# Kernel optimization log

Hardware: AMD Instinct MI355X
Metric: run time of the kernel (lower is better)

The kernel has to match this reference:

```python
import jax, jax.numpy as jnp
import numpy as np

NEG_BIG = -10000000000.0  # value used by masked_fill_ in the original


def setup_inputs() -> dict:
    S, B, H = 2048, 16, 1024
    key = jax.random.key(0)
    ks = jax.random.split(key, 6)
    return {
        "hidden": jax.random.normal(ks[0], (1, B, H), dtype=jnp.float32),
        "hidden_sequence": jax.random.normal(ks[1], (S, B, H), dtype=jnp.float32),
        "input_masks": jax.random.randint(ks[2], (S, B), 0, 2) > 0,
        "W_att": jax.random.normal(ks[3], (H, 2 * H), dtype=jnp.float32) * (1.0 / np.sqrt(2 * H)),
        "b_att": jax.random.normal(ks[4], (H,), dtype=jnp.float32) * 0.01,
        "v": jax.random.normal(ks[5], (H,), dtype=jnp.float32),
    }


def reference(hidden, hidden_sequence, input_masks, W_att, b_att, v):
    S, B, H = hidden_sequence.shape
    # concat score: tanh(Linear([hidden; hidden_seq])) . v  -> [S, B]
    h = jnp.broadcast_to(hidden, (S, B, H))
    concat_hidden = jnp.concatenate([h, hidden_sequence], axis=2)  # [S, B, 2H]
    energy = jnp.tanh(jnp.einsum('sbk,hk->sbh', concat_hidden, W_att) + b_att)
    score = jnp.einsum('sbh,h->sb', energy, v)  # [S, B]
    # masked_fill_(~mask, -1e10); the original's .permute(1,0) result is discarded
    score = jnp.where(input_masks, score, jnp.float32(NEG_BIG))
    # faithful: softmax over dim=1 of the [S, B] energy (as in the source)
    attention_weight = jax.nn.softmax(score, axis=1)  # [S, B]
    # bmm([B,1,S], [B,S,H]) -> [B,1,H] -> permute(1,0,2) -> [1,B,H]
    context = jnp.einsum('sb,sbh->bh', attention_weight, hidden_sequence)[None, :, :]
    return context
```

## Files before the change

### kernel.cpp

```cpp
#include <hip/hip_runtime.h>
#include <math.h>

#define S_LEN 2048
#define B_SZ  16
#define H_SZ  1024
#define M_SZ  32768

typedef __attribute__((ext_vector_type(8))) _Float16 half8;
typedef __attribute__((ext_vector_type(4))) _Float16 half4;
typedef __attribute__((ext_vector_type(4))) float f32x4;

__device__ __forceinline__ unsigned pack2h(float a, float b) {
    _Float16 ha = (_Float16)a, hb = (_Float16)b;
    unsigned short ua = __builtin_bit_cast(unsigned short, ha);
    unsigned short ub = __builtin_bit_cast(unsigned short, hb);
    return (unsigned)ua | ((unsigned)ub << 16);
}

__device__ __forceinline__ float tanh_fast(float x) {
    float e = __expf(2.f * x);
    return __builtin_fmaf(-2.f, __builtin_amdgcn_rcpf(e + 1.f), 1.f);
}

__device__ __forceinline__ int phys_off(int r, int sl) {
    return ((r >> 1) << 7) + ((((r & 1) << 2 | sl) ^ ((r >> 1) & 7)) << 4);
}

__device__ __forceinline__ void dma16(const void* g, void* l) {
    __builtin_amdgcn_global_load_lds(
        (const __attribute__((address_space(1))) unsigned int*)g,
        (__attribute__((address_space(3))) unsigned int*)l, 16, 0, 0);
}

__global__ void k_hidden_part(const float* __restrict__ hidden,
                              const float* __restrict__ W,
                              const float* __restrict__ b_att,
                              float* __restrict__ hp) {
    int gid  = blockIdx.x * blockDim.x + threadIdx.x;
    int wave = gid >> 6;
    int lane = threadIdx.x & 63;
    int b = wave >> 10;
    int h = wave & 1023;
    const float* x = hidden + b * H_SZ;
    const float* w = W + (size_t)h * (2 * H_SZ);
    float acc = 0.f;
    #pragma unroll
    for (int k = 0; k < H_SZ; k += 64) acc += x[k + lane] * w[k + lane];
    #pragma unroll
    for (int off = 32; off; off >>= 1) acc += __shfl_down(acc, off, 64);
    if (lane == 0) hp[b * H_SZ + h] = acc + b_att[h];
}

__global__ void k_conv_tiles(const float* __restrict__ src,
                             unsigned short* __restrict__ dst,
                             int rowStride, int colOff) {
    int t = blockIdx.x * 256 + threadIdx.x;
    int sl = t & 3, r = (t >> 2) & 127, kt = (t >> 9) & 31, p = t >> 14;
    const float* s = src + (size_t)(p * 128 + r) * rowStride + colOff + kt * 32 + sl * 8;
    float4 f0 = *(const float4*)s;
    float4 f1 = *(const float4*)(s + 4);
    uint4 u;
    u.x = pack2h(f0.x, f0.y); u.y = pack2h(f0.z, f0.w);
    u.z = pack2h(f1.x, f1.y); u.w = pack2h(f1.z, f1.w);
    *(uint4*)((char*)dst + (size_t)(p * 32 + kt) * 8192 + phys_off(r, sl)) = u;
}

#define SA2   0
#define SB2   8192
#define SBUF2 16384

__global__ __launch_bounds__(256, 3)
void k_score_pipe(const unsigned short* __restrict__ Xsw,
                  const unsigned short* __restrict__ Wsw,
                  const float* __restrict__ hp,
                  const float* __restrict__ v,
                  float* __restrict__ score_part) {
    __shared__ char lds[3 * SBUF2];

    const int t = threadIdx.x;
    int wg = (blockIdx.x & 7) * 256 + (blockIdx.x >> 3);
    const int mp = wg >> 3;
    const int m0 = mp * 128;
    const int nt = wg & 7;
    const int n0 = nt * 128;

    const int lane = t & 63, wid = t >> 6;
    const int wm = wid >> 1, wn = wid & 1;
    const int lr = lane & 15, lq = lane >> 4;

    const char* At = (const char*)Xsw + (size_t)mp * 32 * 8192 + wid * 1024 + lane * 16;
    const char* Bt = (const char*)Wsw + (size_t)nt * 32 * 8192 + wid * 1024 + lane * 16;

    int aro[4], bro[4];
    #pragma unroll
    for (int i = 0; i < 4; ++i) {
        aro[i] = phys_off(wm * 64 + i * 16 + lr, lq);
        bro[i] = phys_off(wn * 64 + i * 16 + lr, lq);
    }

    f32x4 acc[4][4];
    #pragma unroll
    for (int i = 0; i < 4; ++i)
        #pragma unroll
        for (int j = 0; j < 4; ++j) acc[i][j] = (f32x4)0.f;

#define DMA2(bufbase, kt)                                                      \
    {                                                                          \
        const char* a = At + (size_t)(kt) * 8192;                              \
        const char* b = Bt + (size_t)(kt) * 8192;                              \
        dma16(a,        (bufbase) + SA2 + wid * 1024);                         \
        dma16(a + 4096, (bufbase) + SA2 + 4096 + wid * 1024);                  \
        dma16(b,        (bufbase) + SB2 + wid * 1024);                         \
        dma16(b + 4096, (bufbase) + SB2 + 4096 + wid * 1024);                  \
    }

    char* cb0 = lds;
    char* cb1 = lds + SBUF2;
    char* cb2 = lds + 2 * SBUF2;
    DMA2(cb0, 0);
    DMA2(cb1, 1);

    for (int kt = 0; kt < 32; ++kt) {
        if (kt < 31) { asm volatile("s_waitcnt vmcnt(4)" ::: "memory"); }
        else         { asm volatile("s_waitcnt vmcnt(0)" ::: "memory"); }
        __builtin_amdgcn_s_barrier();
        __builtin_amdgcn_sched_barrier(0);
        if (kt < 30) DMA2(cb2, kt + 2);

        half8 ah[4], bh[4];
        #pragma unroll
        for (int i = 0; i < 4; ++i) ah[i] = *(const half8*)(cb0 + SA2 + aro[i]);
        #pragma unroll
        for (int j = 0; j < 4; ++j) bh[j] = *(const half8*)(cb0 + SB2 + bro[j]);

        __builtin_amdgcn_s_setprio(1);
        #pragma unroll
        for (int i = 0; i < 4; ++i)
            #pragma unroll
            for (int j = 0; j < 4; ++j)
                acc[i][j] = __builtin_amdgcn_mfma_f32_16x16x32_f16(ah[i], bh[j], acc[i][j], 0, 0, 0);
        __builtin_amdgcn_s_setprio(0);

        char* tmp = cb0; cb0 = cb1; cb1 = cb2; cb2 = tmp;
    }
    __syncthreads();

    float* red = (float*)lds;
    #pragma unroll
    for (int i = 0; i < 4; ++i) {
        #pragma unroll
        for (int r = 0; r < 4; ++r) {
            const int b = lq * 4 + r;
            float s = 0.f;
            #pragma unroll
            for (int j = 0; j < 4; ++j) {
                const int c = n0 + wn * 64 + j * 16 + lr;
                s += v[c] * tanh_fast(acc[i][j][r] + hp[b * H_SZ + c]);
            }
            s += __shfl_xor(s, 1);
            s += __shfl_xor(s, 2);
            s += __shfl_xor(s, 4);
            s += __shfl_xor(s, 8);
            if (lr == 0)
                red[wn * 128 + wm * 64 + i * 16 + lq * 4 + r] = s;
        }
    }
    __syncthreads();
    if (t < 128)
        score_part[(size_t)(m0 + t) * 8 + nt] = red[t] + red[128 + t];
#undef DMA2
}

__global__ __launch_bounds__(256, 3)
void k_score_dma(const float* __restrict__ X,
                 const unsigned short* __restrict__ Wsw,
                 const float* __restrict__ hp,
                 const float* __restrict__ v,
                 float* __restrict__ score_part) {
    __shared__ char lds[2 * SBUF2];

    const int t = threadIdx.x;
    int wg = (blockIdx.x & 7) * 256 + (blockIdx.x >> 3);
    const int m0 = (wg >> 3) * 128;
    const int nt = wg & 7;
    const int n0 = nt * 128;

    const int lane = t & 63, wid = t >> 6;
    const int wm = wid >> 1, wn = wid & 1;
    const int lr = lane & 15, lq = lane >> 4;

    const int srow = t >> 1, shalf = t & 1;
    const float* Xp = X + (size_t)(m0 + srow) * 1024 + shalf * 16;
    const int aOff0 = phys_off(srow, shalf * 2 + 0);
    const int aOff1 = phys_off(srow, shalf * 2 + 1);

    const unsigned short* Bp = Wsw + (size_t)(nt * 32) * 4096 + wid * 512 + lane * 8;

    int aro[4], bro[4];
    #pragma unroll
    for (int i = 0; i < 4; ++i) {
        aro[i] = phys_off(wm * 64 + i * 16 + lr, lq);
        bro[i] = phys_off(wn * 64 + i * 16 + lr, lq);
    }

    f32x4 acc[4][4];
    #pragma unroll
    for (int i = 0; i < 4; ++i)
        #pragma unroll
        for (int j = 0; j < 4; ++j) acc[i][j] = (f32x4)0.f;

    float4 ax[4];

#define LOADA(kt)                                                              \
    {                                                                          \
        const float* p = Xp + (kt) * 32;                                       \
        ax[0] = *(const float4*)(p);                                           \
        ax[1] = *(const float4*)(p + 4);                                       \
        ax[2] = *(const float4*)(p + 8);                                       \
        ax[3] = *(const float4*)(p + 12);                                      \
    }

#define DMAB(bufbase, kt)                                                      \
    {                                                                          \
        const unsigned short* s0 = Bp + (size_t)(kt) * 4096;                   \
        dma16(s0,        (bufbase) + SB2 + wid * 1024);                        \
        dma16(s0 + 2048, (bufbase) + SB2 + wid * 1024 + 4096);                 \
    }

#define STAGEA(bufbase)                                                        \
    {                                                                          \
        uint4 p0, p1;                                                          \
        p0.x = pack2h(ax[0].x, ax[0].y); p0.y = pack2h(ax[0].z, ax[0].w);      \
        p0.z = pack2h(ax[1].x, ax[1].y); p0.w = pack2h(ax[1].z, ax[1].w);      \
        p1.x = pack2h(ax[2].x, ax[2].y); p1.y = pack2h(ax[2].z, ax[2].w);      \
        p1.z = pack2h(ax[3].x, ax[3].y); p1.w = pack2h(ax[3].z, ax[3].w);      \
        *(uint4*)((bufbase) + SA2 + aOff0) = p0;                               \
        *(uint4*)((bufbase) + SA2 + aOff1) = p1;                               \
    }

    LOADA(0);
    DMAB(lds, 0);
    STAGEA(lds);
    __syncthreads();

    for (int kt = 0; kt < 32; ++kt) {
        char* cur = lds + (kt & 1) * SBUF2;
        char* nxt = lds + ((kt & 1) ^ 1) * SBUF2;
        if (kt < 31) {
            LOADA(kt + 1);
            DMAB(nxt, kt + 1);
        }

        half8 ah[4], bh[4];
        #pragma unroll
        for (int i = 0; i < 4; ++i) ah[i] = *(const half8*)(cur + SA2 + aro[i]);
        #pragma unroll
        for (int j = 0; j < 4; ++j) bh[j] = *(const half8*)(cur + SB2 + bro[j]);

        #pragma unroll
        for (int i = 0; i < 4; ++i)
            #pragma unroll
            for (int j = 0; j < 4; ++j)
                acc[i][j] = __builtin_amdgcn_mfma_f32_16x16x32_f16(ah[i], bh[j], acc[i][j], 0, 0, 0);

        if (kt < 31) STAGEA(nxt);
        __syncthreads();
    }

    float* red = (float*)lds;
    #pragma unroll
    for (int i = 0; i < 4; ++i) {
        #pragma unroll
        for (int r = 0; r < 4; ++r) {
            const int b = lq * 4 + r;
            float s = 0.f;
            #pragma unroll
            for (int j = 0; j < 4; ++j) {
                const int c = n0 + wn * 64 + j * 16 + lr;
                s += v[c] * tanh_fast(acc[i][j][r] + hp[b * H_SZ + c]);
            }
            s += __shfl_xor(s, 1);
            s += __shfl_xor(s, 2);
            s += __shfl_xor(s, 4);
            s += __shfl_xor(s, 8);
            if (lr == 0)
                red[wn * 128 + wm * 64 + i * 16 + lq * 4 + r] = s;
        }
    }
    __syncthreads();
    if (t < 128)
        score_part[(size_t)(m0 + t) * 8 + nt] = red[t] + red[128 + t];
#undef LOADA
#undef DMAB
#undef STAGEA
}

__global__ void k_softmax(const float* __restrict__ sp,
                          const int* __restrict__ masks,
                          float* __restrict__ wts) {
    int s = blockIdx.x * blockDim.x + threadIdx.x;
    if (s >= S_LEN) return;
    const float4* base = (const float4*)(sp + (size_t)s * 128);
    float vals[16];
    float mx = -INFINITY;
    #pragma unroll
    for (int b = 0; b < 16; ++b) {
        float4 p0 = base[b * 2], p1 = base[b * 2 + 1];
        float sc = ((p0.x + p0.y) + (p0.z + p0.w)) + ((p1.x + p1.y) + (p1.z + p1.w));
        sc = masks[s * 16 + b] ? sc : -1e10f;
        vals[b] = sc;
        mx = fmaxf(mx, sc);
    }
    float sum = 0.f;
    #pragma unroll
    for (int b = 0; b < 16; ++b) { vals[b] = __expf(vals[b] - mx); sum += vals[b]; }
    float inv = 1.f / sum;
    #pragma unroll
    for (int b = 0; b < 16; ++b) wts[s * 16 + b] = vals[b] * inv;
}

__global__ __launch_bounds__(256)
void k_context_f16(const float* __restrict__ wts,
                   const unsigned short* __restrict__ Xsw,
                   float* __restrict__ partial) {
    const int t = threadIdx.x;
    const int b = blockIdx.x & 15;
    const int c = blockIdx.x >> 4;
    const int kt = t >> 3;
    const int sl = (t >> 1) & 3;
    const int e8 = (t & 1) * 8;

    int po[8];
    #pragma unroll
    for (int j = 0; j < 8; ++j) po[j] = phys_off(b + j * 16, sl) + e8;

    const char* base = (const char*)Xsw + ((size_t)(c * 8) * 32 + kt) * 8192;
    float4 acc = make_float4(0.f, 0.f, 0.f, 0.f);
    #pragma unroll
    for (int o = 0; o < 8; ++o) {
        const char* tb = base + (size_t)o * 32 * 8192;
        #pragma unroll
        for (int j = 0; j < 8; ++j) {
            const int s = c * 64 + o * 8 + j;
            float w = wts[s * 16 + b];
            half4 x = *(const half4*)(tb + po[j]);
            acc.x += w * (float)x[0];
            acc.y += w * (float)x[1];
            acc.z += w * (float)x[2];
            acc.w += w * (float)x[3];
        }
    }
    *(float4*)(partial + (size_t)(c * 16 + b) * 1024 + t * 4) = acc;
}

__global__ void k_context_partial(const float* __restrict__ wts,
                                  const float* __restrict__ X,
                                  float* __restrict__ partial) {
    int b = blockIdx.x & 15;
    int c = blockIdx.x >> 4;
    int h = threadIdx.x * 4;
    float4 acc = make_float4(0.f, 0.f, 0.f, 0.f);
    for (int s = c * 64; s < c * 64 + 64; ++s) {
        float w = wts[s * 16 + b];
        float4 x = *(const float4*)(X + (size_t)(s * 16 + b) * 1024 + h);
        acc.x += w * x.x; acc.y += w * x.y; acc.z += w * x.z; acc.w += w * x.w;
    }
    *(float4*)(partial + (size_t)(c * 16 + b) * 1024 + h) = acc;
}

__global__ void k_context_reduce(const float* __restrict__ partial,
                                 float* __restrict__ out) {
    int o = blockIdx.x * blockDim.x + threadIdx.x;
    int b = o >> 10, h = o & 1023;
    float s = 0.f;
    #pragma unroll
    for (int cc = 0; cc < 32; ++cc) s += partial[(size_t)(cc * 16 + b) * 1024 + h];
    out[o] = s;
}

extern "C" void kernel_launch(void* const* d_in, const int* in_sizes, int n_in,
                              void* d_out, int out_size, void* d_ws, size_t ws_size,
                              hipStream_t stream) {
    const float* hidden = (const float*)d_in[0];
    const float* hseq   = (const float*)d_in[1];
    const int*   masks  = (const int*)d_in[2];
    const float* W      = (const float*)d_in[3];
    const float* b_att  = (const float*)d_in[4];
    const float* v      = (const float*)d_in[5];
    float* out = (float*)d_out;

    float* wsf        = (float*)d_ws;
    float* hp         = wsf;
    float* wts        = wsf + 16384;
    float* score_part = wts + 32768;
    float* partial    = score_part + 8 * M_SZ;
    unsigned short* Wsw = (unsigned short*)(partial + 32 * 16 * 1024);
    unsigned short* Xsw = (unsigned short*)((char*)Wsw + 2 * 1024 * 1024);
    const size_t WS_FAST = (size_t)(16384 + 32768 + 262144 + 524288) * 4
                         + 2ull * 1024 * 1024 + 64ull * 1024 * 1024;

    hipLaunchKernelGGL(k_hidden_part, dim3(4096), dim3(256), 0, stream, hidden, W, b_att, hp);
    hipLaunchKernelGGL(k_conv_tiles,  dim3(512),  dim3(256), 0, stream, W, Wsw, 2048, 1024);
    if (ws_size >= WS_FAST) {
        hipLaunchKernelGGL(k_conv_tiles,   dim3(16384), dim3(256), 0, stream, hseq, Xsw, 1024, 0);
        hipLaunchKernelGGL(k_score_pipe,   dim3(2048),  dim3(256), 0, stream, Xsw, Wsw, hp, v, score_part);
        hipLaunchKernelGGL(k_softmax,      dim3(8),     dim3(256), 0, stream, score_part, masks, wts);
        hipLaunchKernelGGL(k_context_f16,  dim3(512),   dim3(256), 0, stream, wts, Xsw, partial);
    } else {
        hipLaunchKernelGGL(k_score_dma,    dim3(2048),  dim3(256), 0, stream, hseq, Wsw, hp, v, score_part);
        hipLaunchKernelGGL(k_softmax,      dim3(8),     dim3(256), 0, stream, score_part, masks, wts);
        hipLaunchKernelGGL(k_context_partial, dim3(512), dim3(256), 0, stream, wts, hseq, partial);
    }
    hipLaunchKernelGGL(k_context_reduce, dim3(64), dim3(256), 0, stream, partial, out);
}
```

Measured before the change: 334.1 us.

## Widen score GEMM tile to 128x256 and fuse W conversion into hidden kernel

The score GEMM now gives each workgroup a 128x256 output tile, with each wave covering all 128 rows and 64 columns. The triple-buffered DMA pipeline loads 24KB per stage, so each A tile is read half as often and the grid shrinks to 1024 blocks. This raises register pressure, and launch bounds drop to 2 blocks per CU. The W-to-fp16 swizzle conversion is folded into the hidden-projection kernel, which removes one launch, and the softmax is adapted to four partial sums per row.

```diff
diff --git a/kernel.cpp b/kernel.cpp
--- a/kernel.cpp
+++ b/kernel.cpp
@@ -32,10 +32,11 @@
         (__attribute__((address_space(3))) unsigned int*)l, 16, 0, 0);
 }
 
-__global__ void k_hidden_part(const float* __restrict__ hidden,
+__global__ void k_hidden_conv(const float* __restrict__ hidden,
                               const float* __restrict__ W,
                               const float* __restrict__ b_att,
-                              float* __restrict__ hp) {
+                              float* __restrict__ hp,
+                              unsigned short* __restrict__ Wsw) {
     int gid  = blockIdx.x * blockDim.x + threadIdx.x;
     int wave = gid >> 6;
     int lane = threadIdx.x & 63;
@@ -49,6 +50,23 @@
     #pragma unroll
     for (int off = 32; off; off >>= 1) acc += __shfl_down(acc, off, 64);
     if (lane == 0) hp[b * H_SZ + h] = acc + b_att[h];
+
+    if (b == 0) {
+        const int p = h >> 7, r = h & 127;
+        const float* src = W + (size_t)h * 2048 + 1024;
+        #pragma unroll
+        for (int q = 0; q < 2; ++q) {
+            int slot = lane + q * 64;
+            int kt = slot >> 2, sl = slot & 3;
+            const float* s8 = src + kt * 32 + sl * 8;
+            float4 f0 = *(const float4*)s8;
+            float4 f1 = *(const float4*)(s8 + 4);
+            uint4 u;
+            u.x = pack2h(f0.x, f0.y); u.y = pack2h(f0.z, f0.w);
+            u.z = pack2h(f1.x, f1.y); u.w = pack2h(f1.z, f1.w);
+            *(uint4*)((char*)Wsw + (size_t)(p * 32 + kt) * 8192 + phys_off(r, sl)) = u;
+        }
+    }
 }
 
 __global__ void k_conv_tiles(const float* __restrict__ src,
@@ -65,42 +83,41 @@
     *(uint4*)((char*)dst + (size_t)(p * 32 + kt) * 8192 + phys_off(r, sl)) = u;
 }
 
-#define SA2   0
-#define SB2   8192
-#define SBUF2 16384
-
-__global__ __launch_bounds__(256, 3)
-void k_score_pipe(const unsigned short* __restrict__ Xsw,
-                  const unsigned short* __restrict__ Wsw,
-                  const float* __restrict__ hp,
-                  const float* __restrict__ v,
-                  float* __restrict__ score_part) {
-    __shared__ char lds[3 * SBUF2];
+#define SBP   8192
+#define PBUF  24576
+
+__global__ __launch_bounds__(256, 2)
+void k_score_pipe2(const unsigned short* __restrict__ Xsw,
+                   const unsigned short* __restrict__ Wsw,
+                   const float* __restrict__ hp,
+                   const float* __restrict__ v,
+                   float* __restrict__ score_part) {
+    __shared__ char lds[3 * PBUF];
 
     const int t = threadIdx.x;
-    int wg = (blockIdx.x & 7) * 256 + (blockIdx.x >> 3);
-    const int mp = wg >> 3;
-    const int m0 = mp * 128;
-    const int nt = wg & 7;
-    const int n0 = nt * 128;
+    int wg = (blockIdx.x & 7) * 128 + (blockIdx.x >> 3);
+    const int mp  = wg >> 2;
+    const int m0  = mp * 128;
+    const int ntq = wg & 3;
+    const int n0  = ntq * 256;
 
     const int lane = t & 63, wid = t >> 6;
-    const int wm = wid >> 1, wn = wid & 1;
     const int lr = lane & 15, lq = lane >> 4;
 
-    const char* At = (const char*)Xsw + (size_t)mp * 32 * 8192 + wid * 1024 + lane * 16;
-    const char* Bt = (const char*)Wsw + (size_t)nt * 32 * 8192 + wid * 1024 + lane * 16;
-
-    int aro[4], bro[4];
-    #pragma unroll
-    for (int i = 0; i < 4; ++i) {
-        aro[i] = phys_off(wm * 64 + i * 16 + lr, lq);
-        bro[i] = phys_off(wn * 64 + i * 16 + lr, lq);
-    }
-
-    f32x4 acc[4][4];
-    #pragma unroll
-    for (int i = 0; i < 4; ++i)
+    const char* At = (const char*)Xsw + (size_t)mp * 32 * 8192 + wid * 2048 + lane * 16;
+    const char* Bt = (const char*)Wsw + (size_t)((ntq * 2 + (wid >> 1)) * 32) * 8192
+                     + (wid & 1) * 4096 + lane * 16;
+
+    int aro[8], bro[4];
+    #pragma unroll
+    for (int i = 0; i < 8; ++i) aro[i] = phys_off(i * 16 + lr, lq);
+    const int bbase = SBP + (wid >> 1) * 8192;
+    #pragma unroll
+    for (int j = 0; j < 4; ++j) bro[j] = bbase + phys_off((wid * 64 + j * 16 + lr) & 127, lq);
+
+    f32x4 acc[8][4];
+    #pragma unroll
+    for (int i = 0; i < 8; ++i)
         #pragma unroll
         for (int j = 0; j < 4; ++j) acc[i][j] = (f32x4)0.f;
 
@@ -108,42 +125,171 @@
     {                                                                          \
         const char* a = At + (size_t)(kt) * 8192;                              \
         const char* b = Bt + (size_t)(kt) * 8192;                              \
-        dma16(a,        (bufbase) + SA2 + wid * 1024);                         \
-        dma16(a + 4096, (bufbase) + SA2 + 4096 + wid * 1024);                  \
-        dma16(b,        (bufbase) + SB2 + wid * 1024);                         \
-        dma16(b + 4096, (bufbase) + SB2 + 4096 + wid * 1024);                  \
+        dma16(a,        (bufbase) + wid * 2048);                               \
+        dma16(a + 1024, (bufbase) + wid * 2048 + 1024);                        \
+        dma16(b,        (bufbase) + SBP + wid * 4096);                         \
+        dma16(b + 1024, (bufbase) + SBP + wid * 4096 + 1024);                  \
+        dma16(b + 2048, (bufbase) + SBP + wid * 4096 + 2048);                  \
+        dma16(b + 3072, (bufbase) + SBP + wid * 4096 + 3072);                  \
     }
 
     char* cb0 = lds;
-    char* cb1 = lds + SBUF2;
-    char* cb2 = lds + 2 * SBUF2;
+    char* cb1 = lds + PBUF;
+    char* cb2 = lds + 2 * PBUF;
     DMA2(cb0, 0);
     DMA2(cb1, 1);
 
     for (int kt = 0; kt < 32; ++kt) {
-        if (kt < 31) { asm volatile("s_waitcnt vmcnt(4)" ::: "memory"); }
+        if (kt < 31) { asm volatile("s_waitcnt vmcnt(6)" ::: "memory"); }
         else         { asm volatile("s_waitcnt vmcnt(0)" ::: "memory"); }
         __builtin_amdgcn_s_barrier();
         __builtin_amdgcn_sched_barrier(0);
         if (kt < 30) DMA2(cb2, kt + 2);
 
+        half8 ah[8], bh[4];
+        #pragma unroll
+        for (int i = 0; i < 8; ++i) ah[i] = *(const half8*)(cb0 + aro[i]);
+        #pragma unroll
+        for (int j = 0; j < 4; ++j) bh[j] = *(const half8*)(cb0 + bro[j]);
+
+        __builtin_amdgcn_s_setprio(1);
+        #pragma unroll
+        for (int i = 0; i < 8; ++i)
+            #pragma unroll
+            for (int j = 0; j < 4; ++j)
+                acc[i][j] = __builtin_amdgcn_mfma_f32_16x16x32_f16(ah[i], bh[j], acc[i][j], 0, 0, 0);
+        __builtin_amdgcn_s_setprio(0);
+
+        char* tmp = cb0; cb0 = cb1; cb1 = cb2; cb2 = tmp;
+    }
+    __syncthreads();
+
+    float* red = (float*)lds;
+    #pragma unroll
+    for (int i = 0; i < 8; ++i) {
+        #pragma unroll
+        for (int r = 0; r < 4; ++r) {
+            const int b = lq * 4 + r;
+            float s = 0.f;
+            #pragma unroll
+            for (int j = 0; j < 4; ++j) {
+                const int c = n0 + wid * 64 + j * 16 + lr;
+                s += v[c] * tanh_fast(acc[i][j][r] + hp[b * H_SZ + c]);
+            }
+            s += __shfl_xor(s, 1);
+            s += __shfl_xor(s, 2);
+            s += __shfl_xor(s, 4);
+            s += __shfl_xor(s, 8);
+            if (lr == 0)
+                red[wid * 128 + i * 16 + lq * 4 + r] = s;
+        }
+    }
+    __syncthreads();
+    if (t < 128)
+        score_part[(size_t)(m0 + t) * 4 + ntq] =
+            red[t] + red[128 + t] + red[256 + t] + red[384 + t];
+#undef DMA2
+}
+
+#define SA2   0
+#define SB2   8192
+#define SBUF2 16384
+
+__global__ __launch_bounds__(256, 3)
+void k_score_dma(const float* __restrict__ X,
+                 const unsigned short* __restrict__ Wsw,
+                 const float* __restrict__ hp,
+                 const float* __restrict__ v,
+                 float* __restrict__ score_part) {
+    __shared__ char lds[2 * SBUF2];
+
+    const int t = threadIdx.x;
+    int wg = (blockIdx.x & 7) * 256 + (blockIdx.x >> 3);
+    const int m0 = (wg >> 3) * 128;
+    const int nt = wg & 7;
+    const int n0 = nt * 128;
+
+    const int lane = t & 63, wid = t >> 6;
+    const int wm = wid >> 1, wn = wid & 1;
+    const int lr = lane & 15, lq = lane >> 4;
+
+    const int srow = t >> 1, shalf = t & 1;
+    const float* Xp = X + (size_t)(m0 + srow) * 1024 + shalf * 16;
+    const int aOff0 = phys_off(srow, shalf * 2 + 0);
+    const int aOff1 = phys_off(srow, shalf * 2 + 1);
+
+    const unsigned short* Bp = Wsw + (size_t)(nt * 32) * 4096 + wid * 512 + lane * 8;
+
+    int aro[4], bro[4];
+    #pragma unroll
+    for (int i = 0; i < 4; ++i) {
+        aro[i] = phys_off(wm * 64 + i * 16 + lr, lq);
+        bro[i] = phys_off(wn * 64 + i * 16 + lr, lq);
+    }
+
+    f32x4 acc[4][4];
+    #pragma unroll
+    for (int i = 0; i < 4; ++i)
+        #pragma unroll
+        for (int j = 0; j < 4; ++j) acc[i][j] = (f32x4)0.f;
+
+    float4 ax[4];
+
+#define LOADA(kt)                                                              \
+    {                                                                          \
+        const float* p = Xp + (kt) * 32;                                       \
+        ax[0] = *(const float4*)(p);                                           \
+        ax[1] = *(const float4*)(p + 4);                                       \
+        ax[2] = *(const float4*)(p + 8);                                       \
+        ax[3] = *(const float4*)(p + 12);                                      \
+    }
+
+#define DMAB(bufbase, kt)                                                      \
+    {                                                                          \
+        const unsigned short* s0 = Bp + (size_t)(kt) * 4096;                   \
+        dma16(s0,        (bufbase) + SB2 + wid * 1024);                        \
+        dma16(s0 + 2048, (bufbase) + SB2 + wid * 1024 + 4096);                 \
+    }
+
+#define STAGEA(bufbase)                                                        \
+    {                                                                          \
+        uint4 p0, p1;                                                          \
+        p0.x = pack2h(ax[0].x, ax[0].y); p0.y = pack2h(ax[0].z, ax[0].w);      \
+        p0.z = pack2h(ax[1].x, ax[1].y); p0.w = pack2h(ax[1].z, ax[1].w);      \
+        p1.x = pack2h(ax[2].x, ax[2].y); p1.y = pack2h(ax[2].z, ax[2].w);      \
+        p1.z = pack2h(ax[3].x, ax[3].y); p1.w = pack2h(ax[3].z, ax[3].w);      \
+        *(uint4*)((bufbase) + SA2 + aOff0) = p0;                               \
+        *(uint4*)((bufbase) + SA2 + aOff1) = p1;                               \
+    }
+
+    LOADA(0);
+    DMAB(lds, 0);
+    STAGEA(lds);
+    __syncthreads();
+
+    for (int kt = 0; kt < 32; ++kt) {
+        char* cur = lds + (kt & 1) * SBUF2;
+        char* nxt = lds + ((kt & 1) ^ 1) * SBUF2;
+        if (kt < 31) {
+            LOADA(kt + 1);
+            DMAB(nxt, kt + 1);
+        }
+
         half8 ah[4], bh[4];
         #pragma unroll
-        for (int i = 0; i < 4; ++i) ah[i] = *(const half8*)(cb0 + SA2 + aro[i]);
-        #pragma unroll
-        for (int j = 0; j < 4; ++j) bh[j] = *(const half8*)(cb0 + SB2 + bro[j]);
-
-        __builtin_amdgcn_s_setprio(1);
+        for (int i = 0; i < 4; ++i) ah[i] = *(const half8*)(cur + SA2 + aro[i]);
+        #pragma unroll
+        for (int j = 0; j < 4; ++j) bh[j] = *(const half8*)(cur + SB2 + bro[j]);
+
         #pragma unroll
         for (int i = 0; i < 4; ++i)
             #pragma unroll
             for (int j = 0; j < 4; ++j)
                 acc[i][j] = __builtin_amdgcn_mfma_f32_16x16x32_f16(ah[i], bh[j], acc[i][j], 0, 0, 0);
-        __builtin_amdgcn_s_setprio(0);
-
-        char* tmp = cb0; cb0 = cb1; cb1 = cb2; cb2 = tmp;
-    }
-    __syncthreads();
+
+        if (kt < 31) STAGEA(nxt);
+        __syncthreads();
+    }
 
     float* red = (float*)lds;
     #pragma unroll
@@ -168,136 +314,38 @@
     __syncthreads();
     if (t < 128)
         score_part[(size_t)(m0 + t) * 8 + nt] = red[t] + red[128 + t];
-#undef DMA2
-}
-
-__global__ __launch_bounds__(256, 3)
-void k_score_dma(const float* __restrict__ X,
-                 const unsigned short* __restrict__ Wsw,
-                 const float* __restrict__ hp,
-                 const float* __restrict__ v,
-                 float* __restrict__ score_part) {
-    __shared__ char lds[2 * SBUF2];
-
-    const int t = threadIdx.x;
-    int wg = (blockIdx.x & 7) * 256 + (blockIdx.x >> 3);
-    const int m0 = (wg >> 3) * 128;
-    const int nt = wg & 7;
-    const int n0 = nt * 128;
-
-    const int lane = t & 63, wid = t >> 6;
-    const int wm = wid >> 1, wn = wid & 1;
-    const int lr = lane & 15, lq = lane >> 4;
-
-    const int srow = t >> 1, shalf = t & 1;
-    const float* Xp = X + (size_t)(m0 + srow) * 1024 + shalf * 16;
-    const int aOff0 = phys_off(srow, shalf * 2 + 0);
-    const int aOff1 = phys_off(srow, shalf * 2 + 1);
-
-    const unsigned short* Bp = Wsw + (size_t)(nt * 32) * 4096 + wid * 512 + lane * 8;
-
-    int aro[4], bro[4];
-    #pragma unroll
-    for (int i = 0; i < 4; ++i) {
-        aro[i] = phys_off(wm * 64 + i * 16 + lr, lq);
-        bro[i] = phys_off(wn * 64 + i * 16 + lr, lq);
-    }
-
-    f32x4 acc[4][4];
-    #pragma unroll
-    for (int i = 0; i < 4; ++i)
-        #pragma unroll
-        for (int j = 0; j < 4; ++j) acc[i][j] = (f32x4)0.f;
-
-    float4 ax[4];
-
-#define LOADA(kt)                                                              \
-    {                                                                          \
-        const float* p = Xp + (kt) * 32;                                       \
-        ax[0] = *(const float4*)(p);                                           \
-        ax[1] = *(const float4*)(p + 4);                                       \
-        ax[2] = *(const float4*)(p + 8);                                       \
-        ax[3] = *(const float4*)(p + 12);                                      \
-    }
-
-#define DMAB(bufbase, kt)                                                      \
-    {                                                                          \
-        const unsigned short* s0 = Bp + (size_t)(kt) * 4096;                   \
-        dma16(s0,        (bufbase) + SB2 + wid * 1024);                        \
-        dma16(s0 + 2048, (bufbase) + SB2 + wid * 1024 + 4096);                 \
-    }
-
-#define STAGEA(bufbase)                                                        \
-    {                                                                          \
-        uint4 p0, p1;                                                          \
-        p0.x = pack2h(ax[0].x, ax[0].y); p0.y = pack2h(ax[0].z, ax[0].w);      \
-        p0.z = pack2h(ax[1].x, ax[1].y); p0.w = pack2h(ax[1].z, ax[1].w);      \
-        p1.x = pack2h(ax[2].x, ax[2].y); p1.y = pack2h(ax[2].z, ax[2].w);      \
-        p1.z = pack2h(ax[3].x, ax[3].y); p1.w = pack2h(ax[3].z, ax[3].w);      \
-        *(uint4*)((bufbase) + SA2 + aOff0) = p0;                               \
-        *(uint4*)((bufbase) + SA2 + aOff1) = p1;                               \
-    }
-
-    LOADA(0);
-    DMAB(lds, 0);
-    STAGEA(lds);
-    __syncthreads();
-
-    for (int kt = 0; kt < 32; ++kt) {
-        char* cur = lds + (kt & 1) * SBUF2;
-        char* nxt = lds + ((kt & 1) ^ 1) * SBUF2;
-        if (kt < 31) {
-            LOADA(kt + 1);
-            DMAB(nxt, kt + 1);
-        }
-
-        half8 ah[4], bh[4];
-        #pragma unroll
-        for (int i = 0; i < 4; ++i) ah[i] = *(const half8*)(cur + SA2 + aro[i]);
-        #pragma unroll
-        for (int j = 0; j < 4; ++j) bh[j] = *(const half8*)(cur + SB2 + bro[j]);
-
-        #pragma unroll
-        for (int i = 0; i < 4; ++i)
-            #pragma unroll
-            for (int j = 0; j < 4; ++j)
-                acc[i][j] = __builtin_amdgcn_mfma_f32_16x16x32_f16(ah[i], bh[j], acc[i][j], 0, 0, 0);
-
-        if (kt < 31) STAGEA(nxt);
-        __syncthreads();
-    }
-
-    float* red = (float*)lds;
-    #pragma unroll
-    for (int i = 0; i < 4; ++i) {
-        #pragma unroll
-        for (int r = 0; r < 4; ++r) {
-            const int b = lq * 4 + r;
-            float s = 0.f;
-            #pragma unroll
-            for (int j = 0; j < 4; ++j) {
-                const int c = n0 + wn * 64 + j * 16 + lr;
-                s += v[c] * tanh_fast(acc[i][j][r] + hp[b * H_SZ + c]);
-            }
-            s += __shfl_xor(s, 1);
-            s += __shfl_xor(s, 2);
-            s += __shfl_xor(s, 4);
-            s += __shfl_xor(s, 8);
-            if (lr == 0)
-                red[wn * 128 + wm * 64 + i * 16 + lq * 4 + r] = s;
-        }
-    }
-    __syncthreads();
-    if (t < 128)
-        score_part[(size_t)(m0 + t) * 8 + nt] = red[t] + red[128 + t];
 #undef LOADA
 #undef DMAB
 #undef STAGEA
 }
 
-__global__ void k_softmax(const float* __restrict__ sp,
-                          const int* __restrict__ masks,
-                          float* __restrict__ wts) {
+__global__ void k_softmax4(const float* __restrict__ sp,
+                           const int* __restrict__ masks,
+                           float* __restrict__ wts) {
+    int s = blockIdx.x * blockDim.x + threadIdx.x;
+    if (s >= S_LEN) return;
+    const float4* base = (const float4*)(sp + (size_t)s * 64);
+    float vals[16];
+    float mx = -INFINITY;
+    #pragma unroll
+    for (int b = 0; b < 16; ++b) {
+        float4 p = base[b];
+        float sc = (p.x + p.y) + (p.z + p.w);
+        sc = masks[s * 16 + b] ? sc : -1e10f;
+        vals[b] = sc;
+        mx = fmaxf(mx, sc);
+    }
+    float sum = 0.f;
+    #pragma unroll
+    for (int b = 0; b < 16; ++b) { vals[b] = __expf(vals[b] - mx); sum += vals[b]; }
+    float inv = 1.f / sum;
+    #pragma unroll
+    for (int b = 0; b < 16; ++b) wts[s * 16 + b] = vals[b] * inv;
+}
+
+__global__ void k_softmax8(const float* __restrict__ sp,
+                           const int* __restrict__ masks,
+                           float* __restrict__ wts) {
     int s = blockIdx.x * blockDim.x + threadIdx.x;
     if (s >= S_LEN) return;
     const float4* base = (const float4*)(sp + (size_t)s * 128);
@@ -399,16 +447,15 @@
     const size_t WS_FAST = (size_t)(16384 + 32768 + 262144 + 524288) * 4
                          + 2ull * 1024 * 1024 + 64ull * 1024 * 1024;
 
-    hipLaunchKernelGGL(k_hidden_part, dim3(4096), dim3(256), 0, stream, hidden, W, b_att, hp);
-    hipLaunchKernelGGL(k_conv_tiles,  dim3(512),  dim3(256), 0, stream, W, Wsw, 2048, 1024);
+    hipLaunchKernelGGL(k_hidden_conv, dim3(4096), dim3(256), 0, stream, hidden, W, b_att, hp, Wsw);
     if (ws_size >= WS_FAST) {
         hipLaunchKernelGGL(k_conv_tiles,   dim3(16384), dim3(256), 0, stream, hseq, Xsw, 1024, 0);
-        hipLaunchKernelGGL(k_score_pipe,   dim3(2048),  dim3(256), 0, stream, Xsw, Wsw, hp, v, score_part);
-        hipLaunchKernelGGL(k_softmax,      dim3(8),     dim3(256), 0, stream, score_part, masks, wts);
+        hipLaunchKernelGGL(k_score_pipe2,  dim3(1024),  dim3(256), 0, stream, Xsw, Wsw, hp, v, score_part);
+        hipLaunchKernelGGL(k_softmax4,     dim3(8),     dim3(256), 0, stream, score_part, masks, wts);
         hipLaunchKernelGGL(k_context_f16,  dim3(512),   dim3(256), 0, stream, wts, Xsw, partial);
     } else {
         hipLaunchKernelGGL(k_score_dma,    dim3(2048),  dim3(256), 0, stream, hseq, Wsw, hp, v, score_part);
-        hipLaunchKernelGGL(k_softmax,      dim3(8),     dim3(256), 0, stream, score_part, masks, wts);
+        hipLaunchKernelGGL(k_softmax8,     dim3(8),     dim3(256), 0, stream, score_part, masks, wts);
         hipLaunchKernelGGL(k_context_partial, dim3(512), dim3(256), 0, stream, wts, hseq, partial);
     }
     hipLaunchKernelGGL(k_context_reduce, dim3(64), dim3(256), 0, stream, partial, out);
```

Measured after the change: 322.1 us. 1.04x faster.
